# Optimization experiments

Hardware: AMD Instinct MI355X
Metric: run time of the kernel (lower is better)

## Reference

```python
import jax, jax.numpy as jnp
import numpy as np

B, N, H, NH, G, L, F = 64, 200, 256, 8, 2, 3, 512
Dh = H // NH


def _ln(x, sb):
    m = x.mean(-1, keepdims=True)
    v = x.var(-1, keepdims=True)
    return (x - m) / jnp.sqrt(v + 1e-5) * sb[0] + sb[1]


def setup_inputs() -> dict:
    key = jax.random.key(0)
    ks = jax.random.split(key, 24)
    rn = lambda k, sh, sc: jax.random.normal(k, sh, jnp.float32) * sc
    s = 1.0 / np.sqrt(H)
    ln_unit = jnp.stack([jnp.ones(H, jnp.float32), jnp.zeros(H, jnp.float32)])
    return {
        "enc_inputs": rn(ks[0], (B, N, H), 1.0),
        "dec_input": rn(ks[1], (B, H), 1.0),
        "dec_h": rn(ks[2], (B, H), 1.0),
        "dec_c": rn(ks[3], (B, H), 1.0),
        "gat_W": rn(ks[4], (G, H, NH * H), s),
        "gat_att_src": rn(ks[5], (G, NH, H), s),
        "gat_att_dst": rn(ks[6], (G, NH, H), s),
        "gat_bias": jnp.zeros((G, H), jnp.float32),
        "gat_ln": ln_unit,
        "enc_attn_W": rn(ks[7], (L, 4, H, H), s),
        "enc_attn_b": jnp.zeros((L, 4, H), jnp.float32),
        "enc_ln1": jnp.broadcast_to(ln_unit, (L, 2, H)),
        "enc_ffn_W1": rn(ks[8], (L, H, F), s),
        "enc_ffn_b1": jnp.zeros((L, F), jnp.float32),
        "enc_ffn_W2": rn(ks[9], (L, F, H), 1.0 / np.sqrt(F)),
        "enc_ffn_b2": jnp.zeros((L, H), jnp.float32),
        "enc_ln2": jnp.broadcast_to(ln_unit, (L, 2, H)),
        "lstm_Wih": rn(ks[10], (4 * H, H), s),
        "lstm_Whh": rn(ks[11], (4 * H, H), s),
        "lstm_b": jnp.zeros((4 * H,), jnp.float32),
        "ptr_Wref": rn(ks[12], (H, H), s),
        "ptr_Wq": rn(ks[13], (H, H), s),
        "ptr_v": rn(ks[14], (H,), s),
        "adj_mask": jax.random.randint(ks[15], (B, N, N), 0, 2, jnp.int32),
        "mask": jax.random.randint(ks[16], (B, N), 0, 2, jnp.int32),
    }


def _forward(enc_inputs, dec_input, dec_h, dec_c, gat_W, gat_att_src, gat_att_dst,
             gat_bias, gat_ln, enc_attn_W, enc_attn_b, enc_ln1, enc_ffn_W1,
             enc_ffn_b1, enc_ffn_W2, enc_ffn_b2, enc_ln2, lstm_Wih, lstm_Whh,
             lstm_b, ptr_Wref, ptr_Wq, ptr_v, adj_mask, mask):
    neg = jnp.float32(-1e9)
    # --- GAT stack (dense masked form of PyG GATConv; edges adj[i,j]: i->j, self-loops added) ---
    eye = jnp.eye(N, dtype=bool)
    A = jnp.where(eye[None], True, adj_mask > 0)  # [B,N,N] src i, tgt j
    Am = jnp.swapaxes(A, 1, 2)[..., None]  # [B, tgt j, src i, 1]
    x = enc_inputs
    for g in range(G):
        xp = (x @ gat_W[g]).reshape(B, N, NH, H)  # per-head transformed feats
        a_src = jnp.einsum('bnhd,hd->bnh', xp, gat_att_src[g])
        a_dst = jnp.einsum('bnhd,hd->bnh', xp, gat_att_dst[g])
        logit = jax.nn.leaky_relu(a_dst[:, :, None, :] + a_src[:, None, :, :], 0.2)
        logit = jnp.where(Am, logit, neg)  # [B,j,i,NH]
        attn = jax.nn.softmax(logit, axis=2)  # softmax over sources i per target j
        msg = jnp.einsum('bjih,bihd->bjhd', attn, xp).mean(axis=2) + gat_bias[g]
        x = x + jax.nn.relu(msg)  # residual per GAT layer
    emb = _ln(enc_inputs + jax.nn.relu(x), gat_ln)
    # --- Transformer encoder layers (masked self-attention, post-LN) ---
    amask = (adj_mask > 0)[:, None]  # [B,1,q,k]
    for l in range(L):
        q = (emb @ enc_attn_W[l, 0] + enc_attn_b[l, 0]).reshape(B, N, NH, Dh)
        k = (emb @ enc_attn_W[l, 1] + enc_attn_b[l, 1]).reshape(B, N, NH, Dh)
        v = (emb @ enc_attn_W[l, 2] + enc_attn_b[l, 2]).reshape(B, N, NH, Dh)
        sc = jnp.einsum('bqhd,bkhd->bhqk', q, k) / np.sqrt(Dh).astype(np.float32)
        sc = jnp.where(amask, sc, neg)
        at = jax.nn.softmax(sc, axis=-1)
        ctx = jnp.einsum('bhqk,bkhd->bqhd', at, v).reshape(B, N, H)
        emb = _ln(emb + ctx @ enc_attn_W[l, 3] + enc_attn_b[l, 3], enc_ln1[l])
        ff = jax.nn.relu(emb @ enc_ffn_W1[l] + enc_ffn_b1[l]) @ enc_ffn_W2[l] + enc_ffn_b2[l]
        emb = _ln(emb + ff, enc_ln2[l])
    # --- LSTM-cell pointer decoder ---
    gates = dec_input @ lstm_Wih.T + dec_h @ lstm_Whh.T + lstm_b
    i_g, f_g, g_g, o_g = jnp.split(gates, 4, axis=-1)
    c = jax.nn.sigmoid(f_g) * dec_c + jax.nn.sigmoid(i_g) * jnp.tanh(g_g)
    h = jax.nn.sigmoid(o_g) * jnp.tanh(c)
    u = jnp.tanh(emb @ ptr_Wref + (h @ ptr_Wq)[:, None, :]) @ ptr_v  # [B,N]
    u = jnp.where(mask > 0, u, neg)
    policy = jax.nn.softmax(u, axis=-1)
    return policy, h, c, emb


def reference(enc_inputs, dec_input, dec_h, dec_c, gat_W, gat_att_src, gat_att_dst,
              gat_bias, gat_ln, enc_attn_W, enc_attn_b, enc_ln1, enc_ffn_W1,
              enc_ffn_b1, enc_ffn_W2, enc_ffn_b2, enc_ln2, lstm_Wih, lstm_Whh,
              lstm_b, ptr_Wref, ptr_Wq, ptr_v, adj_mask, mask):
    return _forward(enc_inputs, dec_input, dec_h, dec_c, gat_W, gat_att_src,
                    gat_att_dst, gat_bias, gat_ln, enc_attn_W, enc_attn_b,
                    enc_ln1, enc_ffn_W1, enc_ffn_b1, enc_ffn_W2, enc_ffn_b2,
                    enc_ln2, lstm_Wih, lstm_Whh, lstm_b, ptr_Wref, ptr_Wq,
                    ptr_v, adj_mask, mask)
```

## Files before the change

kernel.cpp:

```cpp
#include <hip/hip_runtime.h>
#include <cstdio>
#include <math.h>

static constexpr int B_ = 64, N_ = 200, H_ = 256, NH_ = 8, G_ = 2, L_ = 3, F_ = 512;
static constexpr int BN_ = B_ * N_;

typedef unsigned short u16;
typedef __attribute__((ext_vector_type(8))) short short8;
typedef __attribute__((ext_vector_type(4))) float f32x4;

#define LDSP(p) ((__attribute__((address_space(3))) unsigned int*)(p))
#define GLBP(p) ((const __attribute__((address_space(1))) unsigned int*)(p))

__device__ __forceinline__ float wave_sum64(float v) {
#pragma unroll
  for (int off = 32; off; off >>= 1) v += __shfl_xor(v, off);
  return v;
}
__device__ __forceinline__ float sigmoidf_(float x) { return 1.f / (1.f + __expf(-x)); }
__device__ __forceinline__ u16 f2bf(float x) {
  unsigned u = __float_as_uint(x);
  return (u16)((u + 0x7FFFu + ((u >> 16) & 1u)) >> 16);
}
__device__ __forceinline__ float bf2f(u16 x) { return __uint_as_float((unsigned)x << 16); }

template <int ACT, bool HAS_BIAS, bool HAS_RES, bool OUT_BF>
__global__ __launch_bounds__(256) void gemm_bf16(
    const u16* __restrict__ A, const u16* __restrict__ Bt,
    const float* __restrict__ bias, const float* __restrict__ res,
    float* __restrict__ Cf, u16* __restrict__ Cb, int M, int Nn, int K) {
  __shared__ u16 As[128 * 64];
  __shared__ u16 Bs[128 * 64];
  char* asB = (char*)As;
  char* bsB = (char*)Bs;
  const int tid = threadIdx.x;
  const int m0 = blockIdx.x * 128, n0 = blockIdx.y * 128;
  const int lane = tid & 63;
  const int wid = tid >> 6;
  const int wr = (wid >> 1) * 64, wc = (wid & 1) * 64;
  const int Kb = K * 2;
  const char* Ab = (const char*)A + (size_t)m0 * Kb;
  const char* Bb = (const char*)Bt + (size_t)n0 * Kb;
  f32x4 acc[4][4];
#pragma unroll
  for (int i = 0; i < 4; ++i)
#pragma unroll
    for (int j = 0; j < 4; ++j)
#pragma unroll
      for (int r = 0; r < 4; ++r) acc[i][j][r] = 0.f;

  for (int k0 = 0; k0 < K; k0 += 64) {
    if (k0) __syncthreads();
#pragma unroll
    for (int it = 0; it < 4; ++it) {
      const unsigned o = (unsigned)(it * 256 + tid) * 16;
      const int row = o >> 7;
      const unsigned bc = (o & 127u) ^ (unsigned)((row & 7) << 4);
      const unsigned wb = o & ~1023u;
      __builtin_amdgcn_global_load_lds(GLBP(Ab + (size_t)row * Kb + k0 * 2 + bc),
                                       LDSP(asB + wb), 16, 0, 0);
      __builtin_amdgcn_global_load_lds(GLBP(Bb + (size_t)row * Kb + k0 * 2 + bc),
                                       LDSP(bsB + wb), 16, 0, 0);
    }
    __syncthreads();
#pragma unroll
    for (int kk = 0; kk < 2; ++kk) {
      short8 aF[4], bF[4];
#pragma unroll
      for (int i = 0; i < 4; ++i) {
        const int ar = wr + i * 16 + (lane & 15);
        const unsigned ac = (unsigned)(kk * 64 + (lane >> 4) * 16) ^ (unsigned)((ar & 7) << 4);
        aF[i] = *(const short8*)(asB + ar * 128 + ac);
        const int br = wc + i * 16 + (lane & 15);
        const unsigned bc2 = (unsigned)(kk * 64 + (lane >> 4) * 16) ^ (unsigned)((br & 7) << 4);
        bF[i] = *(const short8*)(bsB + br * 128 + bc2);
      }
#pragma unroll
      for (int i = 0; i < 4; ++i)
#pragma unroll
        for (int j = 0; j < 4; ++j)
          acc[i][j] = __builtin_amdgcn_mfma_f32_16x16x32_bf16(aF[i], bF[j], acc[i][j], 0, 0, 0);
    }
  }
#pragma unroll
  for (int i = 0; i < 4; ++i) {
    const int gm0 = m0 + wr + i * 16 + (lane >> 4) * 4;
#pragma unroll
    for (int j = 0; j < 4; ++j) {
      const int gn = n0 + wc + j * 16 + (lane & 15);
      const float bv = HAS_BIAS ? bias[gn] : 0.f;
#pragma unroll
      for (int r = 0; r < 4; ++r) {
        const int gm = gm0 + r;
        float v = acc[i][j][r] + bv;
        if (HAS_RES) v += res[(size_t)gm * Nn + gn];
        if (ACT == 1) v = fmaxf(v, 0.f);
        if (OUT_BF)
          Cb[(size_t)gm * Nn + gn] = f2bf(v);
        else
          Cf[(size_t)gm * Nn + gn] = v;
      }
    }
  }
}

template <int K>
__global__ __launch_bounds__(256) void gemm_ln(
    const u16* __restrict__ A, const u16* __restrict__ Bt,
    const float* __restrict__ bias, const float* __restrict__ res,
    const float* __restrict__ sb, float* __restrict__ out, u16* __restrict__ outB) {
  __shared__ u16 As[64 * 64];
  __shared__ u16 Bs[256 * 64];
  __shared__ float2 red[64][4];
  char* asB = (char*)As;
  char* bsB = (char*)Bs;
  const int tid = threadIdx.x;
  const int m0 = blockIdx.x * 64;
  const int lane = tid & 63, wid = tid >> 6;
  const int wc = wid * 64;
  const int Kb = K * 2;
  const char* Ab = (const char*)A + (size_t)m0 * Kb;
  const char* Bb = (const char*)Bt;
  f32x4 acc[4][4];
#pragma unroll
  for (int i = 0; i < 4; ++i)
#pragma unroll
    for (int j = 0; j < 4; ++j)
#pragma unroll
      for (int r = 0; r < 4; ++r) acc[i][j][r] = 0.f;

  for (int k0 = 0; k0 < K; k0 += 64) {
    if (k0) __syncthreads();
#pragma unroll
    for (int it = 0; it < 2; ++it) {
      const unsigned o = (unsigned)(it * 256 + tid) * 16;
      const int row = o >> 7;
      const unsigned bc = (o & 127u) ^ (unsigned)((row & 7) << 4);
      const unsigned wb = o & ~1023u;
      __builtin_amdgcn_global_load_lds(GLBP(Ab + (size_t)row * Kb + k0 * 2 + bc),
                                       LDSP(asB + wb), 16, 0, 0);
    }
#pragma unroll
    for (int it = 0; it < 8; ++it) {
      const unsigned o = (unsigned)(it * 256 + tid) * 16;
      const int row = o >> 7;
      const unsigned bc = (o & 127u) ^ (unsigned)((row & 7) << 4);
      const unsigned wb = o & ~1023u;
      __builtin_amdgcn_global_load_lds(GLBP(Bb + (size_t)row * Kb + k0 * 2 + bc),
                                       LDSP(bsB + wb), 16, 0, 0);
    }
    __syncthreads();
#pragma unroll
    for (int kk = 0; kk < 2; ++kk) {
      short8 aF[4], bF[4];
#pragma unroll
      for (int i = 0; i < 4; ++i) {
        const int ar = i * 16 + (lane & 15);
        const unsigned ac = (unsigned)(kk * 64 + (lane >> 4) * 16) ^ (unsigned)((ar & 7) << 4);
        aF[i] = *(const short8*)(asB + ar * 128 + ac);
        const int br = wc + i * 16 + (lane & 15);
        const unsigned bc2 = (unsigned)(kk * 64 + (lane >> 4) * 16) ^ (unsigned)((br & 7) << 4);
        bF[i] = *(const short8*)(bsB + br * 128 + bc2);
      }
#pragma unroll
      for (int i = 0; i < 4; ++i)
#pragma unroll
        for (int j = 0; j < 4; ++j)
          acc[i][j] = __builtin_amdgcn_mfma_f32_16x16x32_bf16(aF[i], bF[j], acc[i][j], 0, 0, 0);
    }
  }
#pragma unroll
  for (int i = 0; i < 4; ++i) {
#pragma unroll
    for (int j = 0; j < 4; ++j) {
      const int gn = wc + j * 16 + (lane & 15);
      const float bv = bias[gn];
#pragma unroll
      for (int r = 0; r < 4; ++r) {
        const int gm = m0 + i * 16 + (lane >> 4) * 4 + r;
        acc[i][j][r] += bv + res[(size_t)gm * 256 + gn];
      }
    }
  }
#pragma unroll
  for (int i = 0; i < 4; ++i) {
#pragma unroll
    for (int r = 0; r < 4; ++r) {
      float s = 0.f, q = 0.f;
#pragma unroll
      for (int j = 0; j < 4; ++j) {
        const float v = acc[i][j][r];
        s += v;
        q += v * v;
      }
#pragma unroll
      for (int off = 1; off < 16; off <<= 1) {
        s += __shfl_xor(s, off);
        q += __shfl_xor(q, off);
      }
      if ((lane & 15) == 0) red[i * 16 + (lane >> 4) * 4 + r][wid] = make_float2(s, q);
    }
  }
  __syncthreads();
#pragma unroll
  for (int i = 0; i < 4; ++i) {
#pragma unroll
    for (int r = 0; r < 4; ++r) {
      const int row = i * 16 + (lane >> 4) * 4 + r;
      const float2 p0 = red[row][0], p1 = red[row][1], p2 = red[row][2], p3 = red[row][3];
      const float S = p0.x + p1.x + p2.x + p3.x;
      const float Q = p0.y + p1.y + p2.y + p3.y;
      const float mean = S * (1.f / 256.f);
      const float var = Q * (1.f / 256.f) - mean * mean;
      const float rstd = rsqrtf(var + 1e-5f);
      const int gm = m0 + row;
#pragma unroll
      for (int j = 0; j < 4; ++j) {
        const int gn = wc + j * 16 + (lane & 15);
        const float y = (acc[i][j][r] - mean) * rstd * sb[gn] + sb[256 + gn];
        out[(size_t)gm * 256 + gn] = y;
        outB[(size_t)gm * 256 + gn] = f2bf(y);
      }
    }
  }
}

__global__ __launch_bounds__(256) void gat_projT(
    const u16* __restrict__ Wt, const u16* __restrict__ actB, u16* __restrict__ xpT) {
  __shared__ u16 As[128 * 64];
  __shared__ u16 Bs[128 * 64];
  char* asB = (char*)As;
  char* bsB = (char*)Bs;
  const int tid = threadIdx.x;
  const int m0 = blockIdx.x * 128;
  const int n0 = blockIdx.y * 128;
  const int b = blockIdx.z;
  const int lane = tid & 63;
  const int wid = tid >> 6;
  const int wr = (wid >> 1) * 64, wc = (wid & 1) * 64;
  const char* Ab = (const char*)Wt + (size_t)m0 * 512;
  const char* Bb = (const char*)actB + ((size_t)b * 200 + n0) * 512;
  f32x4 acc[4][4];
#pragma unroll
  for (int i = 0; i < 4; ++i)
#pragma unroll
    for (int j = 0; j < 4; ++j)
#pragma unroll
      for (int r = 0; r < 4; ++r) acc[i][j][r] = 0.f;

  for (int k0 = 0; k0 < 256; k0 += 64) {
    if (k0) __syncthreads();
#pragma unroll
    for (int it = 0; it < 4; ++it) {
      const unsigned o = (unsigned)(it * 256 + tid) * 16;
      const int row = o >> 7;
      const unsigned bc = (o & 127u) ^ (unsigned)((row & 7) << 4);
      const unsigned wb = o & ~1023u;
      __builtin_amdgcn_global_load_lds(GLBP(Ab + (size_t)row * 512 + k0 * 2 + bc),
                                       LDSP(asB + wb), 16, 0, 0);
      __builtin_amdgcn_global_load_lds(GLBP(Bb + (size_t)row * 512 + k0 * 2 + bc),
                                       LDSP(bsB + wb), 16, 0, 0);
    }
    __syncthreads();
#pragma unroll
    for (int kk = 0; kk < 2; ++kk) {
      short8 aF[4], bF[4];
#pragma unroll
      for (int i = 0; i < 4; ++i) {
        const int ar = wr + i * 16 + (lane & 15);
        const unsigned ac = (unsigned)(kk * 64 + (lane >> 4) * 16) ^ (unsigned)((ar & 7) << 4);
        aF[i] = *(const short8*)(asB + ar * 128 + ac);
        const int br = wc + i * 16 + (lane & 15);
        const unsigned bc2 = (unsigned)(kk * 64 + (lane >> 4) * 16) ^ (unsigned)((br & 7) << 4);
        bF[i] = *(const short8*)(bsB + br * 128 + bc2);
      }
#pragma unroll
      for (int i = 0; i < 4; ++i)
#pragma unroll
        for (int j = 0; j < 4; ++j)
          acc[i][j] = __builtin_amdgcn_mfma_f32_16x16x32_bf16(aF[i], bF[j], acc[i][j], 0, 0, 0);
    }
  }
  u16* outb = xpT + (size_t)b * 524288;
#pragma unroll
  for (int i = 0; i < 4; ++i) {
    const int gm0 = m0 + wr + i * 16 + (lane >> 4) * 4;
#pragma unroll
    for (int j = 0; j < 4; ++j) {
      const int gn = n0 + wc + j * 16 + (lane & 15);
#pragma unroll
      for (int r = 0; r < 4; ++r) {
        const int gm = gm0 + r;
        outb[(size_t)gm * 256 + gn] = (gn < N_) ? f2bf(acc[i][j][r]) : (u16)0;
      }
    }
  }
}

__global__ __launch_bounds__(256) void gat_msg_mfma(
    const u16* __restrict__ xpT, const float* __restrict__ asrcH,
    const float4* __restrict__ statsH, const unsigned* __restrict__ adjTW,
    const float* __restrict__ bias, const float* __restrict__ xin,
    float* __restrict__ xout, u16* __restrict__ xoutB) {
  __shared__ u16 Bs[2][256 * 64];
  __shared__ u16 Ps[2][32 * 64];
  const int tid = threadIdx.x;
  const int Lx = blockIdx.x;
  const int xcd = Lx & 7;
  const int slot = Lx >> 3;
  const int q = slot % 7;
  const int b = xcd + 8 * (slot / 7);
  const int m0 = q * 32;
  const int lane = tid & 63, wid = tid >> 6;
  const int wc = wid * 64;
  const char* baseB = (const char*)xpT + ((size_t)b << 20);
  f32x4 acc[2][4];
#pragma unroll
  for (int i = 0; i < 2; ++i)
#pragma unroll
    for (int j = 0; j < 4; ++j)
#pragma unroll
      for (int r = 0; r < 4; ++r) acc[i][j][r] = 0.f;

  auto stageB = [&](int buf, int t) {
    const size_t off = (size_t)(t >> 2) * 131072 + (size_t)((t & 3) * 128);
    char* bD = (char*)Bs[buf];
#pragma unroll
    for (int it = 0; it < 8; ++it) {
      const unsigned o = (unsigned)(it * 256 + tid) * 16;
      const int row = o >> 7;
      const unsigned bc = (o & 127u) ^ (unsigned)((row & 7) << 4);
      const unsigned wb = o & ~1023u;
      __builtin_amdgcn_global_load_lds(GLBP(baseB + off + (size_t)row * 512 + bc),
                                       LDSP(bD + wb), 16, 0, 0);
    }
  };
  auto computeP = [&](int buf, int t) {
    const int h = t >> 2, k0 = (t & 3) * 64;
    const size_t bh8 = ((size_t)(b * 8 + h)) << 8;
    const float* asp = asrcH + bh8 + k0;
    u16* P = Ps[buf];
    const int j = tid >> 3;
    const int ib = (tid & 7) << 3;
    const int gj = m0 + j;
    const int jc = gj < N_ ? gj : N_ - 1;
    const float4 st = statsH[bh8 + jc];
    const unsigned wbits =
        adjTW[((size_t)b * 256 + jc) * 8 + ((k0 + ib) >> 5)] >> ((k0 + ib) & 31);
    const float4 a0 = *(const float4*)(asp + ib);
    const float4 a1 = *(const float4*)(asp + ib + 4);
    const float av[8] = {a0.x, a0.y, a0.z, a0.w, a1.x, a1.y, a1.z, a1.w};
    float pv[8];
#pragma unroll
    for (int u = 0; u < 8; ++u) {
      float x = st.x + av[u];
      x = fmaxf(x, 0.2f * x);
      const float pe = __expf(x - st.y) * st.z;
      pv[u] = ((wbits >> u) & 1u) ? pe : 0.f;
    }
    unsigned pk[4];
#pragma unroll
    for (int qx = 0; qx < 4; ++qx)
      pk[qx] = (unsigned)f2bf(pv[2 * qx]) | ((unsigned)f2bf(pv[2 * qx + 1]) << 16);
    const unsigned ad2 =
        (unsigned)(j * 128) + (((unsigned)(ib * 2)) ^ (((unsigned)(j & 7)) << 4));
    *(uint4*)((char*)P + ad2) = make_uint4(pk[0], pk[1], pk[2], pk[3]);
  };

  stageB(0, 0);
  stageB(1, 1);
  computeP(0, 0);
  asm volatile("s_waitcnt lgkmcnt(0)" ::: "memory");
  asm volatile("s_waitcnt vmcnt(8)" ::: "memory");
  __builtin_amdgcn_s_barrier();

  for (int t = 0; t < 32; ++t) {
    const int cur = t & 1;
    if (t + 1 < 32) computeP(cur ^ 1, t + 1);
    const char* pB = (const char*)Ps[cur];
    const char* bB = (const char*)Bs[cur];
#pragma unroll
    for (int kk = 0; kk < 2; ++kk) {
      short8 aF[2], bF[4];
#pragma unroll
      for (int i = 0; i < 2; ++i) {
        const int ar = i * 16 + (lane & 15);
        const unsigned ac = (unsigned)(kk * 64 + (lane >> 4) * 16) ^ (unsigned)((ar & 7) << 4);
        aF[i] = *(const short8*)(pB + ar * 128 + ac);
      }
#pragma unroll
      for (int j = 0; j < 4; ++j) {
        const int br = wc + j * 16 + (lane & 15);
        const unsigned bc2 = (unsigned)(kk * 64 + (lane >> 4) * 16) ^ (unsigned)((br & 7) << 4);
        bF[j] = *(const short8*)(bB + br * 128 + bc2);
      }
#pragma unroll
      for (int i = 0; i < 2; ++i)
#pragma unroll
        for (int j = 0; j < 4; ++j)
          acc[i][j] = __builtin_amdgcn_mfma_f32_16x16x32_bf16(aF[i], bF[j], acc[i][j], 0, 0, 0);
    }
    asm volatile("s_waitcnt lgkmcnt(0)" ::: "memory");
    __builtin_amdgcn_s_barrier();
    if (t + 2 < 32) {
      stageB(cur, t + 2);
      asm volatile("s_waitcnt vmcnt(8)" ::: "memory");
      __builtin_amdgcn_s_barrier();
    } else if (t + 1 < 32) {
      asm volatile("s_waitcnt vmcnt(0)" ::: "memory");
      __builtin_amdgcn_s_barrier();
    }
  }
#pragma unroll
  for (int i = 0; i < 2; ++i) {
    const int gm0 = m0 + i * 16 + (lane >> 4) * 4;
#pragma unroll
    for (int j = 0; j < 4; ++j) {
      const int gn = wc + j * 16 + (lane & 15);
      const float bv = bias[gn];
#pragma unroll
      for (int r = 0; r < 4; ++r) {
        const int gm = gm0 + r;
        if (gm < N_) {
          const size_t oo = (size_t)(b * N_ + gm) * 256 + gn;
          const float v = xin[oo] + fmaxf(acc[i][j][r] * 0.125f + bv, 0.f);
          xout[oo] = v;
          xoutB[oo] = f2bf(v);
        }
      }
    }
  }
}

__global__ __launch_bounds__(256) void attn_fused(
    const u16* __restrict__ qkvB, const unsigned* __restrict__ adjW,
    u16* __restrict__ ctxB) {
  __shared__ __align__(16) u16 K_lds[208 * 40];
  __shared__ __align__(16) u16 V_lds[32 * 232];
  __shared__ __align__(16) u16 P_lds[4][16 * 232];
  const int Lx = blockIdx.x;
  const int b = (Lx & 7) + 8 * (Lx >> 6);
  const int h = (Lx >> 3) & 7;
  const int tid = threadIdx.x, lane = tid & 63, wid = tid >> 6;
  const u16* qb = qkvB + (size_t)b * 200 * 768;
  for (int e = tid; e < 200 * 32; e += 256) {
    const int kv = e >> 5, d = e & 31;
    K_lds[kv * 40 + d] = qb[(size_t)kv * 768 + 256 + h * 32 + d];
    V_lds[d * 232 + kv] = qb[(size_t)kv * 768 + 512 + h * 32 + d];
  }
  for (int e = tid; e < 32 * 24; e += 256) V_lds[(e / 24) * 232 + 200 + (e % 24)] = 0;
  const int g = lane >> 4, c = lane & 15;
  u16* Pw = P_lds[wid];
  for (int e = lane; e < 16 * 16; e += 64) Pw[(e >> 4) * 232 + 208 + (e & 15)] = 0;
  __syncthreads();
  short8 kf[13];
#pragma unroll
  for (int nt = 0; nt < 13; ++nt)
    kf[nt] = *(const short8*)&K_lds[(nt * 16 + c) * 40 + g * 8];
  const float scale = 0.17677669529663687f;
  for (int t = 0; t < 4; ++t) {
    const int m0 = (wid * 4 + t) * 16;
    int qrow = b * 200 + m0 + c;
    if (qrow > BN_ - 1) qrow = BN_ - 1;
    const short8 qf = *(const short8*)&qkvB[(size_t)qrow * 768 + h * 32 + g * 8];
    f32x4 acc[13];
#pragma unroll
    for (int nt = 0; nt < 13; ++nt) {
      f32x4 z = {0.f, 0.f, 0.f, 0.f};
      acc[nt] = __builtin_amdgcn_mfma_f32_16x16x32_bf16(qf, kf[nt], z, 0, 0, 0);
    }
    unsigned m8[4][8];
#pragma unroll
    for (int r = 0; r < 4; ++r) {
      const uint4* mp = (const uint4*)(adjW + ((size_t)b * 256 + m0 + g * 4 + r) * 8);
      const uint4 a0 = mp[0], a1 = mp[1];
      m8[r][0] = a0.x; m8[r][1] = a0.y; m8[r][2] = a0.z; m8[r][3] = a0.w;
      m8[r][4] = a1.x; m8[r][5] = a1.y; m8[r][6] = a1.z; m8[r][7] = a1.w;
    }
    float mx[4] = {-3e38f, -3e38f, -3e38f, -3e38f};
#pragma unroll
    for (int nt = 0; nt < 13; ++nt) {
      const int col = nt * 16 + c;
      const float sentinel = (col < 200) ? -1e9f : -2e9f;
#pragma unroll
      for (int r = 0; r < 4; ++r) {
        const bool ok = (m8[r][nt >> 1] >> (((nt & 1) << 4) + c)) & 1u;
        const float v = ok ? acc[nt][r] * scale : sentinel;
        acc[nt][r] = v;
        mx[r] = fmaxf(mx[r], v);
      }
    }
#pragma unroll
    for (int off = 1; off < 16; off <<= 1)
#pragma unroll
      for (int r = 0; r < 4; ++r) mx[r] = fmaxf(mx[r], __shfl_xor(mx[r], off));
    float sm[4] = {0.f, 0.f, 0.f, 0.f};
#pragma unroll
    for (int nt = 0; nt < 13; ++nt)
#pragma unroll
      for (int r = 0; r < 4; ++r) {
        const float e = __expf(acc[nt][r] - mx[r]);
        acc[nt][r] = e;
        sm[r] += e;
      }
#pragma unroll
    for (int off = 1; off < 16; off <<= 1)
#pragma unroll
      for (int r = 0; r < 4; ++r) sm[r] += __shfl_xor(sm[r], off);
#pragma unroll
    for (int r = 0; r < 4; ++r) sm[r] = 1.f / sm[r];
#pragma unroll
    for (int nt = 0; nt < 13; ++nt)
#pragma unroll
      for (int r = 0; r < 4; ++r)
        Pw[(g * 4 + r) * 232 + nt * 16 + c] = f2bf(acc[nt][r] * sm[r]);
    f32x4 o0 = {0.f, 0.f, 0.f, 0.f}, o1 = {0.f, 0.f, 0.f, 0.f};
#pragma unroll
    for (int kt = 0; kt < 7; ++kt) {
      const short8 pf = *(const short8*)&Pw[c * 232 + kt * 32 + g * 8];
      const short8 v0 = *(const short8*)&V_lds[c * 232 + kt * 32 + g * 8];
      const short8 v1 = *(const short8*)&V_lds[(16 + c) * 232 + kt * 32 + g * 8];
      o0 = __builtin_amdgcn_mfma_f32_16x16x32_bf16(pf, v0, o0, 0, 0, 0);
      o1 = __builtin_amdgcn_mfma_f32_16x16x32_bf16(pf, v1, o1, 0, 0, 0);
    }
#pragma unroll
    for (int r = 0; r < 4; ++r) {
      const int q = m0 + g * 4 + r;
      if (q < N_) {
        u16* od = ctxB + ((size_t)(b * N_ + q)) * 256 + h * 32;
        od[c] = f2bf(o0[r]);
        od[16 + c] = f2bf(o1[r]);
      }
    }
  }
}

__global__ __launch_bounds__(256) void adj_bits(const int* __restrict__ adj,
                                                unsigned* __restrict__ adjW) {
  const int b = blockIdx.x;
  for (int e = threadIdx.x; e < 256 * 8; e += 256) {
    const int row = e >> 3, w = e & 7;
    unsigned bits = 0u;
    if (row < N_ && w < 7) {
      const int base = w * 32;
      const int lim = (N_ - base) < 32 ? (N_ - base) : 32;
      const int* ar = adj + ((size_t)b * N_ + row) * N_ + base;
      for (int i = 0; i < lim; ++i) bits |= (ar[i] > 0 ? 1u : 0u) << i;
    }
    adjW[((size_t)b * 256 + row) * 8 + w] = bits;
  }
}

__global__ __launch_bounds__(256) void adj_bits2(const int* __restrict__ adjT,
                                                 unsigned* __restrict__ adjTW) {
  const int b = blockIdx.x;
  for (int e = threadIdx.x; e < 256 * 8; e += 256) {
    const int j = e >> 3, w = e & 7;
    unsigned bits = 0u;
    if (j < N_ && w < 7) {
      const int base = w * 32;
      const int lim = (N_ - base) < 32 ? (N_ - base) : 32;
      const int* ar = adjT + ((size_t)b * N_ + j) * N_ + base;
      for (int i = 0; i < lim; ++i) bits |= (ar[i] > 0 ? 1u : 0u) << i;
      if (j >= base && j < base + 32) bits |= 1u << (j - base);
    }
    adjTW[((size_t)b * 256 + j) * 8 + w] = bits;
  }
}

__global__ __launch_bounds__(256) void adj_transpose(const int* __restrict__ adj,
                                                     int* __restrict__ adjT) {
  __shared__ int s[32][33];
  const int b = blockIdx.z;
  const int i0 = blockIdx.x * 32, j0 = blockIdx.y * 32;
  const int tx = threadIdx.x & 31, ty = threadIdx.x >> 5;
#pragma unroll
  for (int u = 0; u < 4; ++u) {
    const int i = i0 + ty + 8 * u, j = j0 + tx;
    if (i < N_ && j < N_) s[ty + 8 * u][tx] = adj[((size_t)b * N_ + i) * N_ + j];
  }
  __syncthreads();
#pragma unroll
  for (int u = 0; u < 4; ++u) {
    const int j = j0 + ty + 8 * u, i = i0 + tx;
    if (i < N_ && j < N_) adjT[((size_t)b * N_ + j) * N_ + i] = s[tx][ty + 8 * u];
  }
}

__device__ const int PREP_TBL[21][6] = {
    {0, 0, 0, 0, 256, 2048},
    {0, 524288, 0, 524288, 256, 2048},
    {1, 0 * 65536, 1, 0, 256, 256},      {1, 1 * 65536, 1, 65536, 256, 256},
    {1, 2 * 65536, 1, 131072, 256, 256}, {1, 4 * 65536, 1, 196608, 256, 256},
    {1, 5 * 65536, 1, 262144, 256, 256}, {1, 6 * 65536, 1, 327680, 256, 256},
    {1, 8 * 65536, 1, 393216, 256, 256}, {1, 9 * 65536, 1, 458752, 256, 256},
    {1, 10 * 65536, 1, 524288, 256, 256},
    {1, 3 * 65536, 2, 0, 256, 256},      {1, 7 * 65536, 2, 65536, 256, 256},
    {1, 11 * 65536, 2, 131072, 256, 256},
    {2, 0, 3, 0, 256, 512}, {2, 131072, 3, 131072, 256, 512}, {2, 262144, 3, 262144, 256, 512},
    {3, 0, 4, 0, 512, 256}, {3, 131072, 4, 131072, 512, 256}, {3, 262144, 4, 262144, 512, 256},
    {4, 0, 5, 0, 256, 256},
};

__global__ __launch_bounds__(256) void prep_weights(
    const float* __restrict__ gat_W, const float* __restrict__ attn_W,
    const float* __restrict__ W1, const float* __restrict__ W2,
    const float* __restrict__ Wref, u16* __restrict__ gatWT, u16* __restrict__ WqkvT,
    u16* __restrict__ WoT, u16* __restrict__ W1T, u16* __restrict__ W2T,
    u16* __restrict__ WrefT) {
  const int mi = blockIdx.y;
  const int R = PREP_TBL[mi][4], C = PREP_TBL[mi][5];
  const int tc = C / 32;
  const int tiles = (R / 32) * tc;
  if ((int)blockIdx.x >= tiles) return;
  const int sel = PREP_TBL[mi][0], dsel = PREP_TBL[mi][2];
  const float* sp = (sel == 0) ? gat_W : (sel == 1) ? attn_W : (sel == 2) ? W1 : (sel == 3) ? W2 : Wref;
  u16* dp = (dsel == 0) ? gatWT : (dsel == 1) ? WqkvT : (dsel == 2) ? WoT : (dsel == 3) ? W1T
            : (dsel == 4) ? W2T : WrefT;
  sp += PREP_TBL[mi][1];
  dp += PREP_TBL[mi][3];
  const int r0 = (blockIdx.x / tc) * 32, c0 = (blockIdx.x % tc) * 32;
  __shared__ float s[32][33];
  const int tx = threadIdx.x & 31, ty = threadIdx.x >> 5;
#pragma unroll
  for (int u = 0; u < 4; ++u) s[ty + 8 * u][tx] = sp[(size_t)(r0 + ty + 8 * u) * C + c0 + tx];
  __syncthreads();
#pragma unroll
  for (int u = 0; u < 4; ++u)
    dp[(size_t)(c0 + ty + 8 * u) * R + r0 + tx] = f2bf(s[tx][ty + 8 * u]);
}

__global__ __launch_bounds__(256) void cast_bf16(const float* __restrict__ in,
                                                 u16* __restrict__ out, int n4) {
  const int i = blockIdx.x * 256 + threadIdx.x;
  if (i >= n4) return;
  const float4 v = ((const float4*)in)[i];
  ushort4 o;
  o.x = f2bf(v.x); o.y = f2bf(v.y); o.z = f2bf(v.z); o.w = f2bf(v.w);
  ((ushort4*)out)[i] = o;
}

__global__ __launch_bounds__(256) void gat_attvec_stats(
    const u16* __restrict__ xpT, const float* __restrict__ att_src,
    const float* __restrict__ att_dst, const unsigned* __restrict__ adjTW,
    float* __restrict__ asrcH, float4* __restrict__ statsH) {
  __shared__ float as_l[256];
  __shared__ float ad_l[256];
  const int bh = blockIdx.x;
  const int b = bh >> 3, h = bh & 7;
  const int i = threadIdx.x;
  const u16* base = xpT + (size_t)bh * 65536 + i;
  const float* vs = att_src + h * 256;
  const float* vd = att_dst + h * 256;
  float ps = 0.f, pd = 0.f;
  for (int d = 0; d < 256; ++d) {
    const float x = bf2f(base[(size_t)d * 256]);
    ps += x * vs[d];
    pd += x * vd[d];
  }
  as_l[i] = ps;
  ad_l[i] = pd;
  asrcH[bh * 256 + i] = ps;
  __syncthreads();
  const int j = i;
  if (j < N_) {
    unsigned wbits[7];
#pragma unroll
    for (int w = 0; w < 7; ++w) wbits[w] = adjTW[((size_t)b * 256 + j) * 8 + w];
    const float ad = ad_l[j];
    float mx = -1e30f;
#pragma unroll
    for (int w = 0; w < 7; ++w) {
      const unsigned bits = wbits[w];
      for (int t = 0; t < 32; ++t) {
        float x = ad + as_l[w * 32 + t];
        x = fmaxf(x, 0.2f * x);
        x = ((bits >> t) & 1u) ? x : -1e9f;
        mx = fmaxf(mx, x);
      }
    }
    float sum = 0.f;
#pragma unroll
    for (int w = 0; w < 7; ++w) {
      const unsigned bits = wbits[w];
      for (int t = 0; t < 32; ++t) {
        float x = ad + as_l[w * 32 + t];
        x = fmaxf(x, 0.2f * x);
        x = ((bits >> t) & 1u) ? x : -1e9f;
        sum += __expf(x - mx);
      }
    }
    statsH[(size_t)bh * 256 + j] = make_float4(ad, mx, 1.f / sum, 0.f);
  }
}

__global__ __launch_bounds__(256) void ln_pre_kernel(
    const float* __restrict__ in1, const float* __restrict__ in2,
    const float* __restrict__ sb, float* __restrict__ out, u16* __restrict__ outB) {
  const int row = blockIdx.x, t = threadIdx.x;
  const long o = (long)row * 256 + t;
  const float v = in1[o] + fmaxf(in2[o], 0.f);
  float s = v, q = v * v;
#pragma unroll
  for (int off = 32; off; off >>= 1) {
    s += __shfl_xor(s, off);
    q += __shfl_xor(q, off);
  }
  __shared__ float sh[8];
  const int wid = t >> 6, lane = t & 63;
  if (lane == 0) {
    sh[wid] = s;
    sh[4 + wid] = q;
  }
  __syncthreads();
  const float S = sh[0] + sh[1] + sh[2] + sh[3];
  const float Q = sh[4] + sh[5] + sh[6] + sh[7];
  const float mean = S * (1.f / 256.f);
  const float var = Q * (1.f / 256.f) - mean * mean;
  const float r = rsqrtf(var + 1e-5f);
  const float y = (v - mean) * r * sb[t] + sb[256 + t];
  out[o] = y;
  outB[o] = f2bf(y);
}

__global__ __launch_bounds__(256) void lstm_gates(
    const float* __restrict__ di, const float* __restrict__ dh,
    const float* __restrict__ Wih, const float* __restrict__ Whh,
    const float* __restrict__ bias, float* __restrict__ gates) {
  const int idx = blockIdx.x * 256 + threadIdx.x;
  const int b = idx >> 10, n = idx & 1023;
  const float4* w1 = (const float4*)(Wih + (size_t)n * 256);
  const float4* w2 = (const float4*)(Whh + (size_t)n * 256);
  const float4* x1 = (const float4*)(di + b * 256);
  const float4* x2 = (const float4*)(dh + b * 256);
  float s = bias[n];
  for (int k = 0; k < 64; ++k) {
    const float4 a = x1[k], wv = w1[k];
    const float4 a2 = x2[k], wv2 = w2[k];
    s += a.x * wv.x + a.y * wv.y + a.z * wv.z + a.w * wv.w;
    s += a2.x * wv2.x + a2.y * wv2.y + a2.z * wv2.z + a2.w * wv2.w;
  }
  gates[idx] = s;
}

__global__ __launch_bounds__(256) void lstm_ew(
    const float* __restrict__ gates, const float* __restrict__ dc,
    float* __restrict__ h_out, float* __restrict__ c_out) {
  const int idx = blockIdx.x * 256 + threadIdx.x;
  const int b = idx >> 8, d = idx & 255;
  const float ig = sigmoidf_(gates[b * 1024 + d]);
  const float fg = sigmoidf_(gates[b * 1024 + 256 + d]);
  const float gg = tanhf(gates[b * 1024 + 512 + d]);
  const float og = sigmoidf_(gates[b * 1024 + 768 + d]);
  const float c = fg * dc[idx] + ig * gg;
  c_out[idx] = c;
  h_out[idx] = og * tanhf(c);
}

__global__ __launch_bounds__(256) void hq_gemm(
    const float* __restrict__ h, const float* __restrict__ Wq, float* __restrict__ hq) {
  const int b = blockIdx.x;
  const int n = threadIdx.x;
  float s = 0.f;
  for (int k = 0; k < 256; ++k) s += h[b * 256 + k] * Wq[k * 256 + n];
  hq[b * 256 + n] = s;
}

__global__ __launch_bounds__(64) void ptr_u(
    const float* __restrict__ pref, const float* __restrict__ hq,
    const float* __restrict__ pv, float* __restrict__ u) {
  const int row = blockIdx.x;
  const int b = row / N_;
  const int lane = threadIdx.x;
  float s = 0.f;
  for (int d = lane; d < 256; d += 64)
    s += tanhf(pref[(long)row * 256 + d] + hq[b * 256 + d]) * pv[d];
  s = wave_sum64(s);
  if (lane == 0) u[row] = s;
}

__global__ __launch_bounds__(256) void policy_softmax(
    const float* __restrict__ u, const int* __restrict__ mask, float* __restrict__ pol) {
  const int b = blockIdx.x, t = threadIdx.x;
  float val = -1e30f;
  if (t < N_) val = (mask[b * N_ + t] > 0) ? u[b * N_ + t] : -1e9f;
  float m = val;
#pragma unroll
  for (int off = 32; off; off >>= 1) m = fmaxf(m, __shfl_xor(m, off));
  __shared__ float sh[8];
  const int wid = t >> 6, lane = t & 63;
  if (lane == 0) sh[wid] = m;
  __syncthreads();
  m = fmaxf(fmaxf(sh[0], sh[1]), fmaxf(sh[2], sh[3]));
  const float e = (t < N_) ? __expf(val - m) : 0.f;
  float s = e;
#pragma unroll
  for (int off = 32; off; off >>= 1) s += __shfl_xor(s, off);
  __syncthreads();
  if (lane == 0) sh[4 + wid] = s;
  __syncthreads();
  const float S = sh[4] + sh[5] + sh[6] + sh[7];
  if (t < N_) pol[b * N_ + t] = e / S;
}

extern "C" void kernel_launch(void* const* d_in, const int* in_sizes, int n_in,
                              void* d_out, int out_size, void* d_ws, size_t ws_size,
                              hipStream_t stream) {
  const float* enc_inputs = (const float*)d_in[0];
  const float* dec_input = (const float*)d_in[1];
  const float* dec_h = (const float*)d_in[2];
  const float* dec_c = (const float*)d_in[3];
  const float* gat_W = (const float*)d_in[4];
  const float* gat_att_src = (const float*)d_in[5];
  const float* gat_att_dst = (const float*)d_in[6];
  const float* gat_bias = (const float*)d_in[7];
  const float* gat_ln = (const float*)d_in[8];
  const float* enc_attn_W = (const float*)d_in[9];
  const float* enc_attn_b = (const float*)d_in[10];
  const float* enc_ln1 = (const float*)d_in[11];
  const float* enc_ffn_W1 = (const float*)d_in[12];
  const float* enc_ffn_b1 = (const float*)d_in[13];
  const float* enc_ffn_W2 = (const float*)d_in[14];
  const float* enc_ffn_b2 = (const float*)d_in[15];
  const float* enc_ln2 = (const float*)d_in[16];
  const float* lstm_Wih = (const float*)d_in[17];
  const float* lstm_Whh = (const float*)d_in[18];
  const float* lstm_b = (const float*)d_in[19];
  const float* ptr_Wref = (const float*)d_in[20];
  const float* ptr_Wq = (const float*)d_in[21];
  const float* ptr_v = (const float*)d_in[22];
  const int* adj = (const int*)d_in[23];
  const int* mask = (const int*)d_in[24];

  float* out = (float*)d_out;
  float* policy = out;
  float* h_out = out + 12800;
  float* c_out = out + 12800 + 16384;
  float* emb = out + 12800 + 16384 + 16384;

  char* ws = (char*)d_ws;
  char* arena = ws;
  size_t o = 134217728;
  float* xbuf = (float*)(ws + o); o += 13107200;
  float* gates = (float*)(ws + o); o += 262144;
  float* hq = (float*)(ws + o); o += 65536;
  float* ubuf = (float*)(ws + o); o += 51200;
  u16* encB = (u16*)(ws + o); o += 6553600;
  u16* xbufB = (u16*)(ws + o); o += 6553600;
  u16* embB = (u16*)(ws + o); o += 6553600;
  int* adjT = (int*)(ws + o); o += 10240000;
  unsigned* adjW = (unsigned*)(ws + o); o += 524288;
  unsigned* adjTW = (unsigned*)(ws + o); o += 524288;
  float* asrcH = (float*)(ws + o); o += 524288;
  float4* statsH = (float4*)(ws + o); o += 2097152;
  u16* gatWT = (u16*)(ws + o); o += 2097152;
  u16* WqkvT = (u16*)(ws + o); o += 1179648;
  u16* WoT = (u16*)(ws + o); o += 393216;
  u16* W1T = (u16*)(ws + o); o += 786432;
  u16* W2T = (u16*)(ws + o); o += 786432;
  u16* WrefT = (u16*)(ws + o); o += 131072;
  if (ws_size < o) fprintf(stderr, "kernel_launch: ws too small (%zu < %zu)\n", ws_size, o);
  u16* xpT = (u16*)arena;
  u16* qkvB = (u16*)arena;
  u16* ctxB = (u16*)(arena + 19660800);
  u16* ffnB = (u16*)(arena + 26214400);
  float* pref = (float*)arena;

  prep_weights<<<dim3(512, 21), 256, 0, stream>>>(gat_W, enc_attn_W, enc_ffn_W1, enc_ffn_W2,
                                                  ptr_Wref, gatWT, WqkvT, WoT, W1T, W2T, WrefT);
  cast_bf16<<<3200, 256, 0, stream>>>(enc_inputs, encB, 819200);
  adj_transpose<<<dim3(7, 7, 64), 256, 0, stream>>>(adj, adjT);
  adj_bits<<<64, 256, 0, stream>>>(adj, adjW);
  adj_bits2<<<64, 256, 0, stream>>>(adjT, adjTW);

  for (int g = 0; g < G_; ++g) {
    const u16* actB = (g == 0) ? encB : xbufB;
    const float* xin = (g == 0) ? enc_inputs : xbuf;
    gat_projT<<<dim3(16, 2, 64), 256, 0, stream>>>(gatWT + (size_t)g * 524288, actB, xpT);
    gat_attvec_stats<<<512, 256, 0, stream>>>(xpT, gat_att_src + g * 2048,
                                              gat_att_dst + g * 2048, adjTW, asrcH, statsH);
    gat_msg_mfma<<<448, 256, 0, stream>>>(xpT, asrcH, statsH, adjTW, gat_bias + g * H_,
                                          xin, xbuf, xbufB);
  }
  ln_pre_kernel<<<BN_, 256, 0, stream>>>(enc_inputs, xbuf, gat_ln, emb, embB);

  for (int l = 0; l < L_; ++l) {
    gemm_bf16<0, true, false, true><<<dim3(100, 6), 256, 0, stream>>>(
        embB, WqkvT + (size_t)l * 196608, enc_attn_b + l * 1024, nullptr, nullptr, qkvB,
        BN_, 768, 256);
    attn_fused<<<512, 256, 0, stream>>>(qkvB, adjW, ctxB);
    gemm_ln<256><<<200, 256, 0, stream>>>(ctxB, WoT + (size_t)l * 65536,
                                          enc_attn_b + l * 1024 + 768, emb,
                                          enc_ln1 + l * 512, emb, embB);
    gemm_bf16<1, true, false, true><<<dim3(100, 4), 256, 0, stream>>>(
        embB, W1T + (size_t)l * 131072, enc_ffn_b1 + l * 512, nullptr, nullptr, ffnB,
        BN_, 512, 256);
    gemm_ln<512><<<200, 256, 0, stream>>>(ffnB, W2T + (size_t)l * 131072,
                                          enc_ffn_b2 + l * 256, emb,
                                          enc_ln2 + l * 512, emb, embB);
  }

  lstm_gates<<<256, 256, 0, stream>>>(dec_input, dec_h, lstm_Wih, lstm_Whh, lstm_b, gates);
  lstm_ew<<<64, 256, 0, stream>>>(gates, dec_c, h_out, c_out);
  hq_gemm<<<64, 256, 0, stream>>>(h_out, ptr_Wq, hq);
  gemm_bf16<0, false, false, false><<<dim3(100, 2), 256, 0, stream>>>(
      embB, WrefT, nullptr, nullptr, pref, nullptr, BN_, 256, 256);
  ptr_u<<<BN_, 64, 0, stream>>>(pref, hq, ptr_v, ubuf);
  policy_softmax<<<B_, 256, 0, stream>>>(ubuf, mask, policy);
}
```

Baseline: 570.7 us.

## Double-buffer gemm_ln K tiles and preload GAT attention stats into registers/LDS

The fused GEMM+LayerNorm kernel now double-buffers its A/B tiles in LDS, so the next K-tile's global-to-LDS loads overlap the current tile's MFMA work instead of running strictly serialized with barriers. The GAT message kernel hoists the per-row stats, adjacency words and source attention scores out of the inner loop: stats and adjacency go into registers once, and the source scores into a shared LDS table, which removes repeated global loads per tile. In exchange LDS use grows, which may lower occupancy, and more registers are held live across the loop.

After: 571.4 us. Within noise of the previous version (+0.1%).

```diff
diff --git a/kernel.cpp b/kernel.cpp
--- a/kernel.cpp
+++ b/kernel.cpp
@@ -109,11 +109,9 @@
     const u16* __restrict__ A, const u16* __restrict__ Bt,
     const float* __restrict__ bias, const float* __restrict__ res,
     const float* __restrict__ sb, float* __restrict__ out, u16* __restrict__ outB) {
-  __shared__ u16 As[64 * 64];
-  __shared__ u16 Bs[256 * 64];
+  __shared__ u16 As[2][64 * 64];
+  __shared__ u16 Bs[2][256 * 64];
   __shared__ float2 red[64][4];
-  char* asB = (char*)As;
-  char* bsB = (char*)Bs;
   const int tid = threadIdx.x;
   const int m0 = blockIdx.x * 64;
   const int lane = tid & 63, wid = tid >> 6;
@@ -121,6 +119,7 @@
   const int Kb = K * 2;
   const char* Ab = (const char*)A + (size_t)m0 * Kb;
   const char* Bb = (const char*)Bt;
+  constexpr int T = K / 64;
   f32x4 acc[4][4];
 #pragma unroll
   for (int i = 0; i < 4; ++i)
@@ -129,8 +128,7 @@
 #pragma unroll
       for (int r = 0; r < 4; ++r) acc[i][j][r] = 0.f;
 
-  for (int k0 = 0; k0 < K; k0 += 64) {
-    if (k0) __syncthreads();
+  auto stage = [&](int buf, int k0) {
 #pragma unroll
     for (int it = 0; it < 2; ++it) {
       const unsigned o = (unsigned)(it * 256 + tid) * 16;
@@ -138,7 +136,7 @@
       const unsigned bc = (o & 127u) ^ (unsigned)((row & 7) << 4);
       const unsigned wb = o & ~1023u;
       __builtin_amdgcn_global_load_lds(GLBP(Ab + (size_t)row * Kb + k0 * 2 + bc),
-                                       LDSP(asB + wb), 16, 0, 0);
+                                       LDSP((char*)As[buf] + wb), 16, 0, 0);
     }
 #pragma unroll
     for (int it = 0; it < 8; ++it) {
@@ -147,9 +145,19 @@
       const unsigned bc = (o & 127u) ^ (unsigned)((row & 7) << 4);
       const unsigned wb = o & ~1023u;
       __builtin_amdgcn_global_load_lds(GLBP(Bb + (size_t)row * Kb + k0 * 2 + bc),
-                                       LDSP(bsB + wb), 16, 0, 0);
-    }
-    __syncthreads();
+                                       LDSP((char*)Bs[buf] + wb), 16, 0, 0);
+    }
+  };
+
+  stage(0, 0);
+  stage(1, 64);
+  asm volatile("s_waitcnt vmcnt(10)" ::: "memory");
+  __builtin_amdgcn_s_barrier();
+
+  for (int t = 0; t < T; ++t) {
+    const int cur = t & 1;
+    const char* asB = (const char*)As[cur];
+    const char* bsB = (const char*)Bs[cur];
 #pragma unroll
     for (int kk = 0; kk < 2; ++kk) {
       short8 aF[4], bF[4];
@@ -167,6 +175,16 @@
 #pragma unroll
         for (int j = 0; j < 4; ++j)
           acc[i][j] = __builtin_amdgcn_mfma_f32_16x16x32_bf16(aF[i], bF[j], acc[i][j], 0, 0, 0);
+    }
+    asm volatile("s_waitcnt lgkmcnt(0)" ::: "memory");
+    __builtin_amdgcn_s_barrier();
+    if (t + 2 < T) {
+      stage(cur, (t + 2) * 64);
+      asm volatile("s_waitcnt vmcnt(10)" ::: "memory");
+      __builtin_amdgcn_s_barrier();
+    } else if (t + 1 < T) {
+      asm volatile("s_waitcnt vmcnt(0)" ::: "memory");
+      __builtin_amdgcn_s_barrier();
     }
   }
 #pragma unroll
@@ -304,6 +322,7 @@
     float* __restrict__ xout, u16* __restrict__ xoutB) {
   __shared__ u16 Bs[2][256 * 64];
   __shared__ u16 Ps[2][32 * 64];
+  __shared__ float asL[8][256];
   const int tid = threadIdx.x;
   const int Lx = blockIdx.x;
   const int xcd = Lx & 7;
@@ -322,6 +341,22 @@
 #pragma unroll
       for (int r = 0; r < 4; ++r) acc[i][j][r] = 0.f;
 
+  const int jrow = tid >> 3;
+  const int ib = (tid & 7) << 3;
+  const int gj = m0 + jrow;
+  const int jc = gj < N_ ? gj : N_ - 1;
+  float4 stR[8];
+#pragma unroll
+  for (int h = 0; h < 8; ++h) stR[h] = statsH[(((size_t)(b * 8 + h)) << 8) + jc];
+  const uint4 aw0 = *(const uint4*)&adjTW[((size_t)b * 256 + jc) * 8];
+  const uint4 aw1 = *(const uint4*)&adjTW[((size_t)b * 256 + jc) * 8 + 4];
+  const unsigned adjR[8] = {aw0.x, aw0.y, aw0.z, aw0.w, aw1.x, aw1.y, aw1.z, aw1.w};
+#pragma unroll
+  for (int e = 0; e < 8; ++e) {
+    const int idx = e * 256 + tid;
+    asL[idx >> 8][idx & 255] = asrcH[((size_t)b * 2048) + idx];
+  }
+
   auto stageB = [&](int buf, int t) {
     const size_t off = (size_t)(t >> 2) * 131072 + (size_t)((t & 3) * 128);
     char* bD = (char*)Bs[buf];
@@ -337,23 +372,13 @@
   };
   auto computeP = [&](int buf, int t) {
     const int h = t >> 2, k0 = (t & 3) * 64;
-    const size_t bh8 = ((size_t)(b * 8 + h)) << 8;
-    const float* asp = asrcH + bh8 + k0;
-    u16* P = Ps[buf];
-    const int j = tid >> 3;
-    const int ib = (tid & 7) << 3;
-    const int gj = m0 + j;
-    const int jc = gj < N_ ? gj : N_ - 1;
-    const float4 st = statsH[bh8 + jc];
-    const unsigned wbits =
-        adjTW[((size_t)b * 256 + jc) * 8 + ((k0 + ib) >> 5)] >> ((k0 + ib) & 31);
-    const float4 a0 = *(const float4*)(asp + ib);
-    const float4 a1 = *(const float4*)(asp + ib + 4);
-    const float av[8] = {a0.x, a0.y, a0.z, a0.w, a1.x, a1.y, a1.z, a1.w};
+    const float4 st = stR[h];
+    const unsigned wbits = adjR[(k0 + ib) >> 5] >> ((k0 + ib) & 31);
+    const float* asp = &asL[h][k0 + ib];
     float pv[8];
 #pragma unroll
     for (int u = 0; u < 8; ++u) {
-      float x = st.x + av[u];
+      float x = st.x + asp[u];
       x = fmaxf(x, 0.2f * x);
       const float pe = __expf(x - st.y) * st.z;
       pv[u] = ((wbits >> u) & 1u) ? pe : 0.f;
@@ -363,12 +388,14 @@
     for (int qx = 0; qx < 4; ++qx)
       pk[qx] = (unsigned)f2bf(pv[2 * qx]) | ((unsigned)f2bf(pv[2 * qx + 1]) << 16);
     const unsigned ad2 =
-        (unsigned)(j * 128) + (((unsigned)(ib * 2)) ^ (((unsigned)(j & 7)) << 4));
-    *(uint4*)((char*)P + ad2) = make_uint4(pk[0], pk[1], pk[2], pk[3]);
+        (unsigned)(jrow * 128) + (((unsigned)(ib * 2)) ^ (((unsigned)(jrow & 7)) << 4));
+    *(uint4*)((char*)Ps[buf] + ad2) = make_uint4(pk[0], pk[1], pk[2], pk[3]);
   };
 
   stageB(0, 0);
   stageB(1, 1);
+  asm volatile("s_waitcnt lgkmcnt(0)" ::: "memory");
+  __builtin_amdgcn_s_barrier();
   computeP(0, 0);
   asm volatile("s_waitcnt lgkmcnt(0)" ::: "memory");
   asm volatile("s_waitcnt vmcnt(8)" ::: "memory");
```

## Double-buffer LDS tiles in gemm_ln to overlap loads with MFMA

Applied to the files above, without the earlier changes.

Converts the gemm_ln K-loop from single-buffered LDS staging to a two-stage ping-pong. The next tile's global_load_lds runs while MFMAs consume the current tile, with explicit vmcnt waits and barriers. The goal is to hide global-load latency behind compute. In exchange, LDS use roughly doubles (about 80KB per block), which may reduce occupancy, and the hand-written waitcnt accounting is fragile.

After: 567.1 us (median of 2 runs). About the same (-0.6%).

```diff
diff --git a/kernel.cpp b/kernel.cpp
--- a/kernel.cpp
+++ b/kernel.cpp
@@ -109,11 +109,9 @@
     const u16* __restrict__ A, const u16* __restrict__ Bt,
     const float* __restrict__ bias, const float* __restrict__ res,
     const float* __restrict__ sb, float* __restrict__ out, u16* __restrict__ outB) {
-  __shared__ u16 As[64 * 64];
-  __shared__ u16 Bs[256 * 64];
+  __shared__ u16 As[2][64 * 64];
+  __shared__ u16 Bs[2][256 * 64];
   __shared__ float2 red[64][4];
-  char* asB = (char*)As;
-  char* bsB = (char*)Bs;
   const int tid = threadIdx.x;
   const int m0 = blockIdx.x * 64;
   const int lane = tid & 63, wid = tid >> 6;
@@ -121,6 +119,7 @@
   const int Kb = K * 2;
   const char* Ab = (const char*)A + (size_t)m0 * Kb;
   const char* Bb = (const char*)Bt;
+  constexpr int T = K / 64;
   f32x4 acc[4][4];
 #pragma unroll
   for (int i = 0; i < 4; ++i)
@@ -129,8 +128,7 @@
 #pragma unroll
       for (int r = 0; r < 4; ++r) acc[i][j][r] = 0.f;
 
-  for (int k0 = 0; k0 < K; k0 += 64) {
-    if (k0) __syncthreads();
+  auto stage = [&](int buf, int k0) {
 #pragma unroll
     for (int it = 0; it < 2; ++it) {
       const unsigned o = (unsigned)(it * 256 + tid) * 16;
@@ -138,7 +136,7 @@
       const unsigned bc = (o & 127u) ^ (unsigned)((row & 7) << 4);
       const unsigned wb = o & ~1023u;
       __builtin_amdgcn_global_load_lds(GLBP(Ab + (size_t)row * Kb + k0 * 2 + bc),
-                                       LDSP(asB + wb), 16, 0, 0);
+                                       LDSP((char*)As[buf] + wb), 16, 0, 0);
     }
 #pragma unroll
     for (int it = 0; it < 8; ++it) {
@@ -147,9 +145,19 @@
       const unsigned bc = (o & 127u) ^ (unsigned)((row & 7) << 4);
       const unsigned wb = o & ~1023u;
       __builtin_amdgcn_global_load_lds(GLBP(Bb + (size_t)row * Kb + k0 * 2 + bc),
-                                       LDSP(bsB + wb), 16, 0, 0);
-    }
-    __syncthreads();
+                                       LDSP((char*)Bs[buf] + wb), 16, 0, 0);
+    }
+  };
+
+  stage(0, 0);
+  stage(1, 64);
+  asm volatile("s_waitcnt vmcnt(10)" ::: "memory");
+  __builtin_amdgcn_s_barrier();
+
+  for (int t = 0; t < T; ++t) {
+    const int cur = t & 1;
+    const char* asB = (const char*)As[cur];
+    const char* bsB = (const char*)Bs[cur];
 #pragma unroll
     for (int kk = 0; kk < 2; ++kk) {
       short8 aF[4], bF[4];
@@ -167,6 +175,16 @@
 #pragma unroll
         for (int j = 0; j < 4; ++j)
           acc[i][j] = __builtin_amdgcn_mfma_f32_16x16x32_bf16(aF[i], bF[j], acc[i][j], 0, 0, 0);
+    }
+    asm volatile("s_waitcnt lgkmcnt(0)" ::: "memory");
+    __builtin_amdgcn_s_barrier();
+    if (t + 2 < T) {
+      stage(cur, (t + 2) * 64);
+      asm volatile("s_waitcnt vmcnt(10)" ::: "memory");
+      __builtin_amdgcn_s_barrier();
+    } else if (t + 1 < T) {
+      asm volatile("s_waitcnt vmcnt(0)" ::: "memory");
+      __builtin_amdgcn_s_barrier();
     }
   }
 #pragma unroll
```
